# Performance work log

Hardware: AMD Instinct MI355X
Metric: run time of the kernel (lower is better)

## Reference

```python
import jax, jax.numpy as jnp
import numpy as np

N_EXPERTS = 8
D_IN = 1024
D_OUT = 1024
BATCH = 4096


def setup_inputs() -> dict:
    key = jax.random.key(0)
    k_x, k_w, k_b, k_a = jax.random.split(key, 4)
    xs = jax.random.normal(k_x, (BATCH, D_IN), dtype=jnp.float32)
    mxs = jnp.arange(BATCH, dtype=jnp.int32)  # opaque per-sample metadata, passed through
    actions = jax.random.randint(k_a, (BATCH,), 0, N_EXPERTS, dtype=jnp.int64)
    # Expert parameters: each submodule is Linear(D_IN -> D_OUT)
    W = jax.random.normal(k_w, (N_EXPERTS, D_OUT, D_IN), dtype=jnp.float32) / np.sqrt(D_IN)
    b = jax.random.normal(k_b, (N_EXPERTS, D_OUT), dtype=jnp.float32) * 0.01
    return {"xs": xs, "mxs": mxs, "actions": actions, "W": W, "b": b}


def reference(xs, mxs, actions, W, b):
    # Original: per-sample python loop y_i = submodule[actions[i]](x_i); cat along batch.
    # Vectorized: compute all experts densely (E small), then select per-sample row.
    y_all = jnp.einsum("bj,eij->bei", xs, W) + b[None, :, :]  # [B, E, D_OUT]
    ys = jnp.take_along_axis(y_all, actions[:, None, None].astype(jnp.int32), axis=1)
    ys = jnp.squeeze(ys, axis=1)  # [B, D_OUT]
    return (ys, mxs, actions)
```

## Files before the change

### kernel.cpp

```cpp
#include <hip/hip_runtime.h>

#define BATCH 4096
#define D_IN 1024
#define D_OUT 1024
#define N_EXPERTS 8

#define TM 64
#define TN 128
#define TK 32
#define MAX_TILES 71

#define WS_PERM    0
#define WS_STARTS  4096
#define WS_TILE_E  4112
#define WS_TILE_M  4200
#define WS_NTILES  4288

#define WS_XHI_OFF   32768
#define WS_XLO_OFF   (32768 + 8388608)
#define WS_WHI_OFF   (32768 + 2*8388608)
#define WS_WLO_OFF   (32768 + 2*8388608 + 16777216)
#define WS_NEEDED    (32768 + 2*8388608 + 2*16777216)

typedef __attribute__((ext_vector_type(8))) short short8;
typedef __attribute__((ext_vector_type(4))) float f32x4;

__device__ __forceinline__ void cvt8(const float4 a, const float4 b,
                                     short8& h, short8& l) {
    float f[8] = {a.x, a.y, a.z, a.w, b.x, b.y, b.z, b.w};
#pragma unroll
    for (int i = 0; i < 8; ++i) {
        const unsigned u = __float_as_uint(f[i]);
        h[i] = (short)(u >> 16);
        const float r = f[i] - __uint_as_float(u & 0xffff0000u);
        l[i] = (short)(__float_as_uint(r) >> 16);
    }
}

__global__ __launch_bounds__(256) void prep_kernel(
    const int* __restrict__ actions, const int* __restrict__ mxs,
    const float* __restrict__ xs, const float* __restrict__ W,
    int* __restrict__ ws,
    short* __restrict__ XhiP, short* __restrict__ XloP,
    short* __restrict__ WhiP, short* __restrict__ WloP,
    float* __restrict__ out, int meta_mode)
{
    const int bid = blockIdx.x;
    const int t = threadIdx.x;

    if (bid == 0) {
        __shared__ int chunkoff[64][N_EXPERTS];
        const int lane = t & 63;
        const int wave = t >> 6;

        for (int it = 0; it < 16; ++it) {
            const int c = wave * 16 + it;
            const int a = actions[c * 64 + lane];
            int myc = 0;
#pragma unroll
            for (int e = 0; e < N_EXPERTS; ++e) {
                const unsigned long long me = __ballot(a == e);
                if (lane == e) myc = (int)__popcll(me);
            }
            if (lane < N_EXPERTS) chunkoff[c][lane] = myc;
        }
        __syncthreads();

        if (wave == 0) {
            int cc0 = chunkoff[lane][0], cc1 = chunkoff[lane][1];
            int cc2 = chunkoff[lane][2], cc3 = chunkoff[lane][3];
            int cc4 = chunkoff[lane][4], cc5 = chunkoff[lane][5];
            int cc6 = chunkoff[lane][6], cc7 = chunkoff[lane][7];
            int tot0, tot1, tot2, tot3, tot4, tot5, tot6, tot7;
            int ex0, ex1, ex2, ex3, ex4, ex5, ex6, ex7;
#define SCAN1(CC, TOT, EX) do {                                   \
            int v = CC;                                           \
            _Pragma("unroll")                                     \
            for (int d = 1; d < 64; d <<= 1) {                    \
                const int u = __shfl_up(v, d, 64);                \
                if (lane >= d) v += u;                            \
            }                                                     \
            TOT = __shfl(v, 63, 64);                              \
            EX = v - CC;                                          \
        } while (0)
            SCAN1(cc0, tot0, ex0); SCAN1(cc1, tot1, ex1);
            SCAN1(cc2, tot2, ex2); SCAN1(cc3, tot3, ex3);
            SCAN1(cc4, tot4, ex4); SCAN1(cc5, tot5, ex5);
            SCAN1(cc6, tot6, ex6); SCAN1(cc7, tot7, ex7);
#undef SCAN1
            const int b0 = 0;
            const int b1 = b0 + tot0, b2 = b1 + tot1, b3 = b2 + tot2;
            const int b4 = b3 + tot3, b5 = b4 + tot4, b6 = b5 + tot5;
            const int b7 = b6 + tot6;
            chunkoff[lane][0] = b0 + ex0; chunkoff[lane][1] = b1 + ex1;
            chunkoff[lane][2] = b2 + ex2; chunkoff[lane][3] = b3 + ex3;
            chunkoff[lane][4] = b4 + ex4; chunkoff[lane][5] = b5 + ex5;
            chunkoff[lane][6] = b6 + ex6; chunkoff[lane][7] = b7 + ex7;
            if (lane == 0) {
                ws[WS_STARTS + 0] = b0; ws[WS_STARTS + 1] = b1;
                ws[WS_STARTS + 2] = b2; ws[WS_STARTS + 3] = b3;
                ws[WS_STARTS + 4] = b4; ws[WS_STARTS + 5] = b5;
                ws[WS_STARTS + 6] = b6; ws[WS_STARTS + 7] = b7;
                ws[WS_STARTS + 8] = BATCH;
                int nt = 0;
                int tots[8] = {tot0, tot1, tot2, tot3, tot4, tot5, tot6, tot7};
#pragma unroll
                for (int e = 0; e < N_EXPERTS; ++e)
                    for (int m0 = 0; m0 < tots[e]; m0 += TM) {
                        ws[WS_TILE_E + nt] = e;
                        ws[WS_TILE_M + nt] = m0;
                        ++nt;
                    }
                ws[WS_NTILES] = nt;
            }
        }
        __syncthreads();

        for (int it = 0; it < 16; ++it) {
            const int c = wave * 16 + it;
            const int i = c * 64 + lane;
            const int a = actions[i];
            unsigned long long msel = 0;
#pragma unroll
            for (int e = 0; e < N_EXPERTS; ++e) {
                const unsigned long long me = __ballot(a == e);
                if (a == e) msel = me;
            }
            const int rank = (int)__popcll(msel & ((1ull << lane) - 1ull));
            const int pos = chunkoff[c][a] + rank;
            ws[WS_PERM + pos] = i;
        }
        return;
    }

    if (bid <= 16) {
        const int i = (bid - 1) * 256 + t;
        if (meta_mode == 2) {
            out[BATCH * D_OUT + i] = (float)mxs[i];
            long long* a64 = (long long*)(out + BATCH * D_OUT + BATCH);
            a64[i] = (long long)actions[i];
        } else if (meta_mode == 1) {
            out[BATCH * D_OUT + i] = (float)mxs[i];
            out[BATCH * D_OUT + BATCH + i] = (float)actions[i];
        }
        return;
    }

    const int g = (bid - 17) * 256 + t;
    if (g < 1048576) {
        const int slot = g & 63;
        const int i2   = (g >> 6) & 7;
        const int blk  = g >> 9;
        const int nt   = blk & 7;
        const int kt   = (blk >> 3) & 31;
        const int e    = blk >> 8;
        const int c    = slot & 15;
        const int j    = slot >> 4;
        const int n    = nt * 128 + i2 * 16 + c;
        const float* p = W + ((size_t)(e << 10) + n) * D_IN + kt * 32 + j * 8;
        const float4 f0 = *(const float4*)p;
        const float4 f1 = *(const float4*)(p + 4);
        short8 h, l;
        cvt8(f0, f1, h, l);
        *(short8*)(WhiP + (size_t)g * 8) = h;
        *(short8*)(WloP + (size_t)g * 8) = l;
    } else {
        const int g2 = g - 1048576;
        const float* p = xs + (size_t)g2 * 8;
        const float4 f0 = *(const float4*)p;
        const float4 f1 = *(const float4*)(p + 4);
        short8 h, l;
        cvt8(f0, f1, h, l);
        *(short8*)(XhiP + (size_t)g2 * 8) = h;
        *(short8*)(XloP + (size_t)g2 * 8) = l;
    }
}

__global__ __launch_bounds__(256) void moe_gemm_pc(
    const short* __restrict__ Xhi, const short* __restrict__ Xlo,
    const short* __restrict__ Whi, const short* __restrict__ Wlo,
    const float* __restrict__ bias, const int* __restrict__ ws,
    float* __restrict__ out)
{
    const int wid = blockIdx.x;
    const int nsl = wid & 7;
    const int tix = wid >> 3;
    if (tix >= ws[WS_NTILES]) return;
    const int e   = ws[WS_TILE_E + tix];
    const int m0  = ws[WS_TILE_M + tix];
    const int s0  = ws[WS_STARTS + e];
    const int cnt = ws[WS_STARTS + e + 1] - s0;
    const int n0  = nsl * TN;

    __shared__ short Ahi[2][4 * 512];
    __shared__ short Alo[2][4 * 512];
    __shared__ short Bhi[2][8 * 512];
    __shared__ short Blo[2][8 * 512];
    __shared__ int   rows_s[TM];

    const int t = threadIdx.x;
    if (t < TM) {
        const int r = m0 + t;
        rows_s[t] = (r < cnt) ? ws[WS_PERM + s0 + r] : -1;
    }
    __syncthreads();

    const int lane = t & 63;
    const int wave = t >> 6;
    const int wm = (wave & 1) * 32;
    const int wn = (wave >> 1) * 64;

    const float zf = 0.f;
    f32x4 acc[2][4];
#pragma unroll
    for (int mi = 0; mi < 2; ++mi)
#pragma unroll
        for (int nj = 0; nj < 4; ++nj)
            acc[mi][nj] = (f32x4){zf, zf, zf, zf};

    const int arow0 = rows_s[wave * 16 + (lane & 15)];
    const int arow  = arow0 < 0 ? 0 : arow0;
    const short* aSrcHi = Xhi + (size_t)arow * D_IN + (lane >> 4) * 8;
    const short* aSrcLo = Xlo + (size_t)arow * D_IN + (lane >> 4) * 8;

    const size_t wBase = ((size_t)e * 256 + (size_t)nsl) * 4096;
    const size_t bo0 = (size_t)wave * 512 + lane * 8;
    const size_t bo1 = (size_t)(wave + 4) * 512 + lane * 8;

#define STAGE(KT, BUF) do {                                                    \
        const int _kt = (KT);                                                  \
        __builtin_amdgcn_global_load_lds(                                      \
            (const __attribute__((address_space(1))) void*)(aSrcHi + _kt * 32),\
            (__attribute__((address_space(3))) void*)&Ahi[BUF][wave * 512],    \
            16, 0, 0);                                                         \
        __builtin_amdgcn_global_load_lds(                                      \
            (const __attribute__((address_space(1))) void*)(aSrcLo + _kt * 32),\
            (__attribute__((address_space(3))) void*)&Alo[BUF][wave * 512],    \
            16, 0, 0);                                                         \
        {                                                                      \
            const size_t _wo = wBase + (size_t)_kt * 32768;                    \
            __builtin_amdgcn_global_load_lds(                                  \
                (const __attribute__((address_space(1))) void*)(Whi + _wo + bo0), \
                (__attribute__((address_space(3))) void*)&Bhi[BUF][wave * 512],\
                16, 0, 0);                                                     \
            __builtin_amdgcn_global_load_lds(                                  \
                (const __attribute__((address_space(1))) void*)(Wlo + _wo + bo0), \
                (__attribute__((address_space(3))) void*)&Blo[BUF][wave * 512],\
                16, 0, 0);                                                     \
            __builtin_amdgcn_global_load_lds(                                  \
                (const __attribute__((address_space(1))) void*)(Whi + _wo + bo1), \
                (__attribute__((address_space(3))) void*)&Bhi[BUF][(wave + 4) * 512], \
                16, 0, 0);                                                     \
            __builtin_amdgcn_global_load_lds(                                  \
                (const __attribute__((address_space(1))) void*)(Wlo + _wo + bo1), \
                (__attribute__((address_space(3))) void*)&Blo[BUF][(wave + 4) * 512], \
                16, 0, 0);                                                     \
        }                                                                      \
    } while (0)

    const int rds = lane * 8;

#define FRAG_MFMA(BUF) do {                                                  \
        short8 ah[2], al[2], bh[4], bl[4];                                   \
        _Pragma("unroll")                                                    \
        for (int i2 = 0; i2 < 2; ++i2) {                                     \
            const int aoff = ((wm >> 4) + i2) * 512 + rds;                   \
            ah[i2] = *(const short8*)&Ahi[BUF][aoff];                        \
            al[i2] = *(const short8*)&Alo[BUF][aoff];                        \
        }                                                                    \
        _Pragma("unroll")                                                    \
        for (int i2 = 0; i2 < 4; ++i2) {                                     \
            const int boff = ((wn >> 4) + i2) * 512 + rds;                   \
            bh[i2] = *(const short8*)&Bhi[BUF][boff];                        \
            bl[i2] = *(const short8*)&Blo[BUF][boff];                        \
        }                                                                    \
        _Pragma("unroll")                                                    \
        for (int mi = 0; mi < 2; ++mi)                                       \
            _Pragma("unroll")                                                \
            for (int nj = 0; nj < 4; ++nj) {                                 \
                acc[mi][nj] = __builtin_amdgcn_mfma_f32_16x16x32_bf16(ah[mi], bh[nj], acc[mi][nj], 0, 0, 0); \
                acc[mi][nj] = __builtin_amdgcn_mfma_f32_16x16x32_bf16(ah[mi], bl[nj], acc[mi][nj], 0, 0, 0); \
                acc[mi][nj] = __builtin_amdgcn_mfma_f32_16x16x32_bf16(al[mi], bh[nj], acc[mi][nj], 0, 0, 0); \
            }                                                                \
    } while (0)

#define WAIT6_BAR() asm volatile("s_waitcnt vmcnt(6)\n\ts_barrier" ::: "memory")
#define WAIT0_BAR() asm volatile("s_waitcnt vmcnt(0)\n\ts_barrier" ::: "memory")
#define READ_FENCE() asm volatile("s_waitcnt lgkmcnt(0)\n\ts_barrier" ::: "memory")

    STAGE(0, 0);
    STAGE(1, 1);

    int kt = 2;
#pragma unroll 1
    for (int i = 0; i < 15; ++i) {
        WAIT6_BAR();
        FRAG_MFMA(0);
        READ_FENCE();
        STAGE(kt, 0);
        WAIT6_BAR();
        FRAG_MFMA(1);
        READ_FENCE();
        STAGE(kt + 1, 1);
        kt += 2;
    }
    WAIT6_BAR();
    FRAG_MFMA(0);
    WAIT0_BAR();
    FRAG_MFMA(1);

#undef STAGE
#undef FRAG_MFMA
#undef WAIT6_BAR
#undef WAIT0_BAR
#undef READ_FENCE

    const int cl = lane & 15;
    const int qd = lane >> 4;
    float bv[4];
#pragma unroll
    for (int nj = 0; nj < 4; ++nj)
        bv[nj] = bias[e * D_OUT + n0 + wn + nj * 16 + cl];
#pragma unroll
    for (int mi = 0; mi < 2; ++mi) {
#pragma unroll
        for (int reg = 0; reg < 4; ++reg) {
            const int mloc = wm + mi * 16 + qd * 4 + reg;
            const int r = rows_s[mloc];
            if (r >= 0) {
                float* orow = out + (size_t)r * D_OUT + n0 + wn + cl;
#pragma unroll
                for (int nj = 0; nj < 4; ++nj)
                    orow[nj * 16] = acc[mi][nj][reg] + bv[nj];
            }
        }
    }
}

__global__ __launch_bounds__(256) void moe_gemm_fb(
    const float* __restrict__ xs, const float* __restrict__ W,
    const float* __restrict__ bias, const int* __restrict__ ws,
    float* __restrict__ out)
{
    const int tix = blockIdx.y;
    if (tix >= ws[WS_NTILES]) return;
    const int e   = ws[WS_TILE_E + tix];
    const int m0  = ws[WS_TILE_M + tix];
    const int s0  = ws[WS_STARTS + e];
    const int cnt = ws[WS_STARTS + e + 1] - s0;
    const int n0  = blockIdx.x * TN;

    __shared__ short Ahi[2][TM * TK];
    __shared__ short Alo[2][TM * TK];
    __shared__ short Bhi[2][TN * TK];
    __shared__ short Blo[2][TN * TK];
    __shared__ int   rows_s[TM];

    const int t = threadIdx.x;
    if (t < TM) {
        const int r = m0 + t;
        rows_s[t] = (r < cnt) ? ws[WS_PERM + s0 + r] : -1;
    }
    __syncthreads();

    const int lane = t & 63;
    const int wave = t >> 6;
    const int wm = (wave & 1) * 32;
    const int wn = (wave >> 1) * 64;

    const float zf = 0.f;
    f32x4 acc[2][4];
#pragma unroll
    for (int mi = 0; mi < 2; ++mi)
#pragma unroll
        for (int nj = 0; nj < 4; ++nj)
            acc[mi][nj] = (f32x4){zf, zf, zf, zf};

    const float* Wb = W + (size_t)e * (D_OUT * (size_t)D_IN) + (size_t)n0 * D_IN;

    const int j  = t & 3;
    const int rr = t >> 2;

    const int arow = rows_s[rr];
    const float* aptr = (arow >= 0) ? (xs + (size_t)arow * D_IN + j * 8) : nullptr;

    const int slotA   = (j * 16 + (rr & 15)) ^ (j << 1);
    const int aoff_st = (rr >> 4) * 512 + slotA * 8;
    const int boff0   = aoff_st;
    const int boff1   = aoff_st + 4 * 512;

    const float* qb0 = Wb + (size_t)rr * D_IN + j * 8;
    const float* qb1 = Wb + (size_t)(64 + rr) * D_IN + j * 8;

    const int rds = (lane ^ ((lane >> 4) << 1)) * 8;

#define LOAD_SET(A0, A1, B0, B1, B2, B3, KOFF) do {                          \
        const int _k = (KOFF);                                               \
        if (aptr) {                                                          \
            A0 = *(const float4*)(aptr + _k);                                \
            A1 = *(const float4*)(aptr + _k + 4);                            \
        }                                                                    \
        B0 = *(const float4*)(qb0 + _k); B1 = *(const float4*)(qb0 + _k + 4);\
        B2 = *(const float4*)(qb1 + _k); B3 = *(const float4*)(qb1 + _k + 4);\
    } while (0)

#define CVT_STORE_SET(A0, A1, B0, B1, B2, B3, BUF) do {                      \
        short8 _h, _l;                                                       \
        cvt8(A0, A1, _h, _l);                                                \
        *(short8*)&Ahi[BUF][aoff_st] = _h; *(short8*)&Alo[BUF][aoff_st] = _l;\
        cvt8(B0, B1, _h, _l);                                                \
        *(short8*)&Bhi[BUF][boff0] = _h;   *(short8*)&Blo[BUF][boff0] = _l;  \
        cvt8(B2, B3, _h, _l);                                                \
        *(short8*)&Bhi[BUF][boff1] = _h;   *(short8*)&Blo[BUF][boff1] = _l;  \
    } while (0)

#define FRAG_MFMA(BUF) do {                                                  \
        short8 ah[2], al[2], bh[4], bl[4];                                   \
        _Pragma("unroll")                                                    \
        for (int i2 = 0; i2 < 2; ++i2) {                                     \
            const int aoff = ((wm >> 4) + i2) * 512 + rds;                   \
            ah[i2] = *(const short8*)&Ahi[BUF][aoff];                        \
            al[i2] = *(const short8*)&Alo[BUF][aoff];                        \
        }                                                                    \
        _Pragma("unroll")                                                    \
        for (int i2 = 0; i2 < 4; ++i2) {                                     \
            const int boff = ((wn >> 4) + i2) * 512 + rds;                   \
            bh[i2] = *(const short8*)&Bhi[BUF][boff];                        \
            bl[i2] = *(const short8*)&Blo[BUF][boff];                        \
        }                                                                    \
        _Pragma("unroll")                                                    \
        for (int mi = 0; mi < 2; ++mi)                                       \
            _Pragma("unroll")                                                \
            for (int nj = 0; nj < 4; ++nj) {                                 \
                acc[mi][nj] = __builtin_amdgcn_mfma_f32_16x16x32_bf16(ah[mi], bh[nj], acc[mi][nj], 0, 0, 0); \
                acc[mi][nj] = __builtin_amdgcn_mfma_f32_16x16x32_bf16(ah[mi], bl[nj], acc[mi][nj], 0, 0, 0); \
                acc[mi][nj] = __builtin_amdgcn_mfma_f32_16x16x32_bf16(al[mi], bh[nj], acc[mi][nj], 0, 0, 0); \
            }                                                                \
    } while (0)

#define PIPE_BARRIER() asm volatile("s_waitcnt lgkmcnt(0)\n\ts_barrier" ::: "memory")

    float4 ax0 = make_float4(0.f, 0.f, 0.f, 0.f), ax1 = ax0;
    float4 bx0, bx1, bx2, bx3;
    float4 ay0 = make_float4(0.f, 0.f, 0.f, 0.f), ay1 = ay0;
    float4 by0, by1, by2, by3;

    LOAD_SET(ax0, ax1, bx0, bx1, bx2, bx3, 0);
    CVT_STORE_SET(ax0, ax1, bx0, bx1, bx2, bx3, 0);
    LOAD_SET(ax0, ax1, bx0, bx1, bx2, bx3, TK);
    PIPE_BARRIER();

    int ke = 2 * TK;
#pragma unroll 1
    for (int i = 0; i < 15; ++i) {
        {
            LOAD_SET(ay0, ay1, by0, by1, by2, by3, ke);
            FRAG_MFMA(0);
            CVT_STORE_SET(ax0, ax1, bx0, bx1, bx2, bx3, 1);
            PIPE_BARRIER();
        }
        {
            LOAD_SET(ax0, ax1, bx0, bx1, bx2, bx3, ke + TK);
            FRAG_MFMA(1);
            CVT_STORE_SET(ay0, ay1, by0, by1, by2, by3, 0);
            PIPE_BARRIER();
        }
        ke += 2 * TK;
    }
    {
        FRAG_MFMA(0);
        CVT_STORE_SET(ax0, ax1, bx0, bx1, bx2, bx3, 1);
        PIPE_BARRIER();
    }
    {
        FRAG_MFMA(1);
    }

#undef LOAD_SET
#undef CVT_STORE_SET
#undef FRAG_MFMA
#undef PIPE_BARRIER

    const int cl = lane & 15;
    const int qd = lane >> 4;
    float bv[4];
#pragma unroll
    for (int nj = 0; nj < 4; ++nj)
        bv[nj] = bias[e * D_OUT + n0 + wn + nj * 16 + cl];
#pragma unroll
    for (int mi = 0; mi < 2; ++mi) {
#pragma unroll
        for (int reg = 0; reg < 4; ++reg) {
            const int mloc = wm + mi * 16 + qd * 4 + reg;
            const int r = rows_s[mloc];
            if (r >= 0) {
                float* orow = out + (size_t)r * D_OUT + n0 + wn + cl;
#pragma unroll
                for (int nj = 0; nj < 4; ++nj)
                    orow[nj * 16] = acc[mi][nj][reg] + bv[nj];
            }
        }
    }
}

extern "C" void kernel_launch(void* const* d_in, const int* in_sizes, int n_in,
                              void* d_out, int out_size, void* d_ws, size_t ws_size,
                              hipStream_t stream) {
    const float* xs      = (const float*)d_in[0];
    const int*   mxs     = (const int*)d_in[1];
    const int*   actions = (const int*)d_in[2];
    const float* W       = (const float*)d_in[3];
    const float* bias    = (const float*)d_in[4];
    float* out = (float*)d_out;
    int*   ws  = (int*)d_ws;
    char*  wsb = (char*)d_ws;

    short* XhiP = (short*)(wsb + WS_XHI_OFF);
    short* XloP = (short*)(wsb + WS_XLO_OFF);
    short* WhiP = (short*)(wsb + WS_WHI_OFF);
    short* WloP = (short*)(wsb + WS_WLO_OFF);

    const int metaOff = BATCH * D_OUT;
    const int meta_mode = (out_size >= metaOff + 3 * BATCH) ? 2
                        : (out_size >= metaOff + 2 * BATCH) ? 1 : 0;

    const bool big = ws_size >= (size_t)WS_NEEDED;
    const int prep_blocks = big ? (17 + 6144) : 17;

    prep_kernel<<<prep_blocks, 256, 0, stream>>>(
        actions, mxs, xs, W, ws, XhiP, XloP, WhiP, WloP, out, meta_mode);

    if (big) {
        moe_gemm_pc<<<8 * MAX_TILES, 256, 0, stream>>>(XhiP, XloP, WhiP, WloP, bias, ws, out);
    } else {
        dim3 grid(D_OUT / TN, MAX_TILES, 1);
        moe_gemm_fb<<<grid, 256, 0, stream>>>(xs, W, bias, ws, out);
    }
}
```

Baseline: 152.7 us.

## Enlarge MoE GEMM tiles to 128x128 with 512-thread blocks and XCD-aware mapping

The precomputed-split GEMM moves from 64x128 tiles with 256 threads to 128x128 tiles with 8 waves, so each block reuses every W tile across twice as many rows. Tile lists are built with a runtime tile height, and each wave now issues one B load per stage instead of two, with the vmcnt wait adjusted to match. Block indices are remapped so that consecutive tiles spread across XCDs while N-slices of one tile stay on the same XCD. In exchange there are fewer blocks and more padding waste on partially filled expert tiles, and the larger blocks need more LDS.

```diff
diff --git a/kernel.cpp b/kernel.cpp
--- a/kernel.cpp
+++ b/kernel.cpp
@@ -5,10 +5,9 @@
 #define D_OUT 1024
 #define N_EXPERTS 8
 
-#define TM 64
-#define TN 128
 #define TK 32
 #define MAX_TILES 71
+#define MAX_TILES_128 39
 
 #define WS_PERM    0
 #define WS_STARTS  4096
@@ -43,7 +42,7 @@
     int* __restrict__ ws,
     short* __restrict__ XhiP, short* __restrict__ XloP,
     short* __restrict__ WhiP, short* __restrict__ WloP,
-    float* __restrict__ out, int meta_mode)
+    float* __restrict__ out, int meta_mode, int tm_tile)
 {
     const int bid = blockIdx.x;
     const int t = threadIdx.x;
@@ -106,7 +105,7 @@
                 int tots[8] = {tot0, tot1, tot2, tot3, tot4, tot5, tot6, tot7};
 #pragma unroll
                 for (int e = 0; e < N_EXPERTS; ++e)
-                    for (int m0 = 0; m0 < tots[e]; m0 += TM) {
+                    for (int m0 = 0; m0 < tots[e]; m0 += tm_tile) {
                         ws[WS_TILE_E + nt] = e;
                         ws[WS_TILE_M + nt] = m0;
                         ++nt;
@@ -176,30 +175,35 @@
     }
 }
 
-__global__ __launch_bounds__(256) void moe_gemm_pc(
+#define TM5 128
+#define TN5 128
+
+__global__ __launch_bounds__(512) void moe_gemm_pc(
     const short* __restrict__ Xhi, const short* __restrict__ Xlo,
     const short* __restrict__ Whi, const short* __restrict__ Wlo,
     const float* __restrict__ bias, const int* __restrict__ ws,
     float* __restrict__ out)
 {
     const int wid = blockIdx.x;
-    const int nsl = wid & 7;
-    const int tix = wid >> 3;
+    const int xcd = wid & 7;
+    const int j5  = wid >> 3;
+    const int nsl = j5 & 7;
+    const int tix = (j5 >> 3) * 8 + xcd;
     if (tix >= ws[WS_NTILES]) return;
     const int e   = ws[WS_TILE_E + tix];
     const int m0  = ws[WS_TILE_M + tix];
     const int s0  = ws[WS_STARTS + e];
     const int cnt = ws[WS_STARTS + e + 1] - s0;
-    const int n0  = nsl * TN;
-
-    __shared__ short Ahi[2][4 * 512];
-    __shared__ short Alo[2][4 * 512];
+    const int n0  = nsl * TN5;
+
+    __shared__ short Ahi[2][8 * 512];
+    __shared__ short Alo[2][8 * 512];
     __shared__ short Bhi[2][8 * 512];
     __shared__ short Blo[2][8 * 512];
-    __shared__ int   rows_s[TM];
+    __shared__ int   rows_s[TM5];
 
     const int t = threadIdx.x;
-    if (t < TM) {
+    if (t < TM5) {
         const int r = m0 + t;
         rows_s[t] = (r < cnt) ? ws[WS_PERM + s0 + r] : -1;
     }
@@ -207,8 +211,8 @@
 
     const int lane = t & 63;
     const int wave = t >> 6;
-    const int wm = (wave & 1) * 32;
-    const int wn = (wave >> 1) * 64;
+    const int wm = (wave >> 1) * 32;
+    const int wn = (wave & 1) * 64;
 
     const float zf = 0.f;
     f32x4 acc[2][4];
@@ -224,8 +228,7 @@
     const short* aSrcLo = Xlo + (size_t)arow * D_IN + (lane >> 4) * 8;
 
     const size_t wBase = ((size_t)e * 256 + (size_t)nsl) * 4096;
-    const size_t bo0 = (size_t)wave * 512 + lane * 8;
-    const size_t bo1 = (size_t)(wave + 4) * 512 + lane * 8;
+    const size_t bo = (size_t)wave * 512 + lane * 8;
 
 #define STAGE(KT, BUF) do {                                                    \
         const int _kt = (KT);                                                  \
@@ -240,20 +243,12 @@
         {                                                                      \
             const size_t _wo = wBase + (size_t)_kt * 32768;                    \
             __builtin_amdgcn_global_load_lds(                                  \
-                (const __attribute__((address_space(1))) void*)(Whi + _wo + bo0), \
+                (const __attribute__((address_space(1))) void*)(Whi + _wo + bo), \
                 (__attribute__((address_space(3))) void*)&Bhi[BUF][wave * 512],\
                 16, 0, 0);                                                     \
             __builtin_amdgcn_global_load_lds(                                  \
-                (const __attribute__((address_space(1))) void*)(Wlo + _wo + bo0), \
+                (const __attribute__((address_space(1))) void*)(Wlo + _wo + bo), \
                 (__attribute__((address_space(3))) void*)&Blo[BUF][wave * 512],\
-                16, 0, 0);                                                     \
-            __builtin_amdgcn_global_load_lds(                                  \
-                (const __attribute__((address_space(1))) void*)(Whi + _wo + bo1), \
-                (__attribute__((address_space(3))) void*)&Bhi[BUF][(wave + 4) * 512], \
-                16, 0, 0);                                                     \
-            __builtin_amdgcn_global_load_lds(                                  \
-                (const __attribute__((address_space(1))) void*)(Wlo + _wo + bo1), \
-                (__attribute__((address_space(3))) void*)&Blo[BUF][(wave + 4) * 512], \
                 16, 0, 0);                                                     \
         }                                                                      \
     } while (0)
@@ -284,7 +279,7 @@
             }                                                                \
     } while (0)
 
-#define WAIT6_BAR() asm volatile("s_waitcnt vmcnt(6)\n\ts_barrier" ::: "memory")
+#define WAIT4_BAR() asm volatile("s_waitcnt vmcnt(4)\n\ts_barrier" ::: "memory")
 #define WAIT0_BAR() asm volatile("s_waitcnt vmcnt(0)\n\ts_barrier" ::: "memory")
 #define READ_FENCE() asm volatile("s_waitcnt lgkmcnt(0)\n\ts_barrier" ::: "memory")
 
@@ -294,24 +289,24 @@
     int kt = 2;
 #pragma unroll 1
     for (int i = 0; i < 15; ++i) {
-        WAIT6_BAR();
+        WAIT4_BAR();
         FRAG_MFMA(0);
         READ_FENCE();
         STAGE(kt, 0);
-        WAIT6_BAR();
+        WAIT4_BAR();
         FRAG_MFMA(1);
         READ_FENCE();
         STAGE(kt + 1, 1);
         kt += 2;
     }
-    WAIT6_BAR();
+    WAIT4_BAR();
     FRAG_MFMA(0);
     WAIT0_BAR();
     FRAG_MFMA(1);
 
 #undef STAGE
 #undef FRAG_MFMA
-#undef WAIT6_BAR
+#undef WAIT4_BAR
 #undef WAIT0_BAR
 #undef READ_FENCE
 
@@ -336,6 +331,9 @@
         }
     }
 }
+
+#define TMF 64
+#define TNF 128
 
 __global__ __launch_bounds__(256) void moe_gemm_fb(
     const float* __restrict__ xs, const float* __restrict__ W,
@@ -348,16 +346,16 @@
     const int m0  = ws[WS_TILE_M + tix];
     const int s0  = ws[WS_STARTS + e];
     const int cnt = ws[WS_STARTS + e + 1] - s0;
-    const int n0  = blockIdx.x * TN;
-
-    __shared__ short Ahi[2][TM * TK];
-    __shared__ short Alo[2][TM * TK];
-    __shared__ short Bhi[2][TN * TK];
-    __shared__ short Blo[2][TN * TK];
-    __shared__ int   rows_s[TM];
+    const int n0  = blockIdx.x * TNF;
+
+    __shared__ short Ahi[2][TMF * TK];
+    __shared__ short Alo[2][TMF * TK];
+    __shared__ short Bhi[2][TNF * TK];
+    __shared__ short Blo[2][TNF * TK];
+    __shared__ int   rows_s[TMF];
 
     const int t = threadIdx.x;
-    if (t < TM) {
+    if (t < TMF) {
         const int r = m0 + t;
         rows_s[t] = (r < cnt) ? ws[WS_PERM + s0 + r] : -1;
     }
@@ -526,14 +524,16 @@
 
     const bool big = ws_size >= (size_t)WS_NEEDED;
     const int prep_blocks = big ? (17 + 6144) : 17;
+    const int tm_tile = big ? TM5 : TMF;
 
     prep_kernel<<<prep_blocks, 256, 0, stream>>>(
-        actions, mxs, xs, W, ws, XhiP, XloP, WhiP, WloP, out, meta_mode);
+        actions, mxs, xs, W, ws, XhiP, XloP, WhiP, WloP, out, meta_mode, tm_tile);
 
     if (big) {
-        moe_gemm_pc<<<8 * MAX_TILES, 256, 0, stream>>>(XhiP, XloP, WhiP, WloP, bias, ws, out);
+        moe_gemm_pc<<<8 * (MAX_TILES_128 + 1), 512, 0, stream>>>(
+            XhiP, XloP, WhiP, WloP, bias, ws, out);
     } else {
-        dim3 grid(D_OUT / TN, MAX_TILES, 1);
+        dim3 grid(D_OUT / TNF, MAX_TILES, 1);
         moe_gemm_fb<<<grid, 256, 0, stream>>>(xs, W, bias, ws, out);
     }
 }
```

Measured after the change: 147.8 us. -3.3%, faster.

## Triple-buffer LDS stages in precomputed MoE GEMM with one barrier per K-step

Applied to the files above, without the earlier changes.

The bf16-split GEMM kernel moves from double to triple LDS buffering. Each K-step now does a single combined wait-and-barrier, then issues the global-to-LDS stage two steps ahead, then runs the MFMAs. This replaces the previous pattern of two barriers per step and lets the next tile's loads overlap the current compute. The cost is about 1.5x more shared memory per block, which may lower occupancy. Tile constants are renamed and the tile table offsets are enlarged, but this does not change behaviour.

```diff
diff --git a/kernel.cpp b/kernel.cpp
--- a/kernel.cpp
+++ b/kernel.cpp
@@ -5,16 +5,14 @@
 #define D_OUT 1024
 #define N_EXPERTS 8
 
-#define TM 64
-#define TN 128
 #define TK 32
 #define MAX_TILES 71
 
 #define WS_PERM    0
 #define WS_STARTS  4096
 #define WS_TILE_E  4112
-#define WS_TILE_M  4200
-#define WS_NTILES  4288
+#define WS_TILE_M  4280
+#define WS_NTILES  4448
 
 #define WS_XHI_OFF   32768
 #define WS_XLO_OFF   (32768 + 8388608)
@@ -43,7 +41,7 @@
     int* __restrict__ ws,
     short* __restrict__ XhiP, short* __restrict__ XloP,
     short* __restrict__ WhiP, short* __restrict__ WloP,
-    float* __restrict__ out, int meta_mode)
+    float* __restrict__ out, int meta_mode, int tm_tile)
 {
     const int bid = blockIdx.x;
     const int t = threadIdx.x;
@@ -106,7 +104,7 @@
                 int tots[8] = {tot0, tot1, tot2, tot3, tot4, tot5, tot6, tot7};
 #pragma unroll
                 for (int e = 0; e < N_EXPERTS; ++e)
-                    for (int m0 = 0; m0 < tots[e]; m0 += TM) {
+                    for (int m0 = 0; m0 < tots[e]; m0 += tm_tile) {
                         ws[WS_TILE_E + nt] = e;
                         ws[WS_TILE_M + nt] = m0;
                         ++nt;
@@ -176,6 +174,9 @@
     }
 }
 
+#define TM9 64
+#define TN9 128
+
 __global__ __launch_bounds__(256) void moe_gemm_pc(
     const short* __restrict__ Xhi, const short* __restrict__ Xlo,
     const short* __restrict__ Whi, const short* __restrict__ Wlo,
@@ -190,16 +191,16 @@
     const int m0  = ws[WS_TILE_M + tix];
     const int s0  = ws[WS_STARTS + e];
     const int cnt = ws[WS_STARTS + e + 1] - s0;
-    const int n0  = nsl * TN;
-
-    __shared__ short Ahi[2][4 * 512];
-    __shared__ short Alo[2][4 * 512];
-    __shared__ short Bhi[2][8 * 512];
-    __shared__ short Blo[2][8 * 512];
-    __shared__ int   rows_s[TM];
+    const int n0  = nsl * TN9;
+
+    __shared__ short Ahi[3][4 * 512];
+    __shared__ short Alo[3][4 * 512];
+    __shared__ short Bhi[3][8 * 512];
+    __shared__ short Blo[3][8 * 512];
+    __shared__ int   rows_s[TM9];
 
     const int t = threadIdx.x;
-    if (t < TM) {
+    if (t < TM9) {
         const int r = m0 + t;
         rows_s[t] = (r < cnt) ? ws[WS_PERM + s0 + r] : -1;
     }
@@ -284,36 +285,27 @@
             }                                                                \
     } while (0)
 
-#define WAIT6_BAR() asm volatile("s_waitcnt vmcnt(6)\n\ts_barrier" ::: "memory")
-#define WAIT0_BAR() asm volatile("s_waitcnt vmcnt(0)\n\ts_barrier" ::: "memory")
-#define READ_FENCE() asm volatile("s_waitcnt lgkmcnt(0)\n\ts_barrier" ::: "memory")
+#define WAIT6_BAR() asm volatile("s_waitcnt vmcnt(6) lgkmcnt(0)\n\ts_barrier" ::: "memory")
+#define WAIT0_BAR() asm volatile("s_waitcnt vmcnt(0) lgkmcnt(0)\n\ts_barrier" ::: "memory")
 
     STAGE(0, 0);
     STAGE(1, 1);
 
     int kt = 2;
 #pragma unroll 1
-    for (int i = 0; i < 15; ++i) {
-        WAIT6_BAR();
-        FRAG_MFMA(0);
-        READ_FENCE();
-        STAGE(kt, 0);
-        WAIT6_BAR();
-        FRAG_MFMA(1);
-        READ_FENCE();
-        STAGE(kt + 1, 1);
-        kt += 2;
-    }
-    WAIT6_BAR();
-    FRAG_MFMA(0);
-    WAIT0_BAR();
-    FRAG_MFMA(1);
+    for (int i = 0; i < 10; ++i) {
+        WAIT6_BAR(); STAGE(kt,     2); FRAG_MFMA(0);
+        WAIT6_BAR(); STAGE(kt + 1, 0); FRAG_MFMA(1);
+        WAIT6_BAR(); STAGE(kt + 2, 1); FRAG_MFMA(2);
+        kt += 3;
+    }
+    WAIT6_BAR(); FRAG_MFMA(0);
+    WAIT0_BAR(); FRAG_MFMA(1);
 
 #undef STAGE
 #undef FRAG_MFMA
 #undef WAIT6_BAR
 #undef WAIT0_BAR
-#undef READ_FENCE
 
     const int cl = lane & 15;
     const int qd = lane >> 4;
@@ -336,6 +328,9 @@
         }
     }
 }
+
+#define TMF 64
+#define TNF 128
 
 __global__ __launch_bounds__(256) void moe_gemm_fb(
     const float* __restrict__ xs, const float* __restrict__ W,
@@ -348,16 +343,16 @@
     const int m0  = ws[WS_TILE_M + tix];
     const int s0  = ws[WS_STARTS + e];
     const int cnt = ws[WS_STARTS + e + 1] - s0;
-    const int n0  = blockIdx.x * TN;
-
-    __shared__ short Ahi[2][TM * TK];
-    __shared__ short Alo[2][TM * TK];
-    __shared__ short Bhi[2][TN * TK];
-    __shared__ short Blo[2][TN * TK];
-    __shared__ int   rows_s[TM];
+    const int n0  = blockIdx.x * TNF;
+
+    __shared__ short Ahi[2][TMF * TK];
+    __shared__ short Alo[2][TMF * TK];
+    __shared__ short Bhi[2][TNF * TK];
+    __shared__ short Blo[2][TNF * TK];
+    __shared__ int   rows_s[TMF];
 
     const int t = threadIdx.x;
-    if (t < TM) {
+    if (t < TMF) {
         const int r = m0 + t;
         rows_s[t] = (r < cnt) ? ws[WS_PERM + s0 + r] : -1;
     }
@@ -528,12 +523,13 @@
     const int prep_blocks = big ? (17 + 6144) : 17;
 
     prep_kernel<<<prep_blocks, 256, 0, stream>>>(
-        actions, mxs, xs, W, ws, XhiP, XloP, WhiP, WloP, out, meta_mode);
+        actions, mxs, xs, W, ws, XhiP, XloP, WhiP, WloP, out, meta_mode, TM9);
 
     if (big) {
-        moe_gemm_pc<<<8 * MAX_TILES, 256, 0, stream>>>(XhiP, XloP, WhiP, WloP, bias, ws, out);
+        moe_gemm_pc<<<8 * MAX_TILES, 256, 0, stream>>>(
+            XhiP, XloP, WhiP, WloP, bias, ws, out);
     } else {
-        dim3 grid(D_OUT / TN, MAX_TILES, 1);
+        dim3 grid(D_OUT / TNF, MAX_TILES, 1);
         moe_gemm_fb<<<grid, 256, 0, stream>>>(xs, W, bias, ws, out);
     }
 }
```

New measurement: 169.9 us. 1.11x slower.
